# Optimization experiments

Hardware: AMD Instinct MI355X
Metric: run time of the kernel (lower is better)

The kernel has to match this reference:

```python
import jax, jax.numpy as jnp
import numpy as np

N, E, D = 100000, 1600000, 128
BN_EPS = 1e-5


def setup_inputs() -> dict:
    key = jax.random.key(0)
    k0, k1, k2 = jax.random.split(key, 3)
    x = jax.random.normal(k0, (N, D), dtype=jnp.float32)
    edge_index = jax.random.randint(k1, (2, E), 0, N, dtype=jnp.int32)
    # GCNConv weight (glorot-ish scale) and bias
    W = jax.random.normal(k2, (D, D), dtype=jnp.float32) * (1.0 / np.sqrt(D))
    b = jnp.zeros((D,), dtype=jnp.float32)
    # BatchNorm1d affine params
    gamma = jnp.ones((D,), dtype=jnp.float32)
    beta = jnp.zeros((D,), dtype=jnp.float32)
    # PReLU single shared slope (torch default init 0.25)
    a_prelu = jnp.asarray(0.25, dtype=jnp.float32)
    return {"x": x, "W": W, "b": b, "gamma": gamma, "beta": beta,
            "a_prelu": a_prelu, "edge_index": edge_index}


def reference(x, W, b, gamma, beta, a_prelu, edge_index):
    n = x.shape[0]
    loops = jnp.arange(n, dtype=edge_index.dtype)
    src = jnp.concatenate([edge_index[0], loops])  # [E+N]
    dst = jnp.concatenate([edge_index[1], loops])  # [E+N]

    # GCN symmetric normalization with self-loops: deg counts incoming edges
    deg = jax.ops.segment_sum(jnp.ones_like(dst, dtype=x.dtype), dst, num_segments=n)
    dinv = jax.lax.rsqrt(deg)  # deg >= 1 thanks to self-loops
    enorm = dinv[src] * dinv[dst]  # [E+N]

    xw = x @ W                                        # [N, D] transform first
    msg = xw[src] * enorm[:, None]                    # gather + scale
    out = jax.ops.segment_sum(msg, dst, num_segments=n) + b  # scatter-add

    # BatchNorm1d over nodes (training-mode batch statistics, biased var)
    mean = jnp.mean(out, axis=0)
    var = jnp.mean(jnp.square(out - mean), axis=0)
    out = (out - mean) * jax.lax.rsqrt(var + BN_EPS) * gamma + beta

    # PReLU (single shared slope); dropout is identity in eval mode
    out = jnp.where(out > 0, out, a_prelu * out)

    # identity residual (in_dim == out_dim)
    return out + x
```

## Files before the change

kernel.cpp:

```cpp
#include <hip/hip_runtime.h>

#define DIM 128
#define BSH 7
#define BUCK 128
#define CAP2 3072
#define CSH 11
#define CPB 16
#define BINCH 2048
#define MAXC 128

typedef __attribute__((ext_vector_type(8))) short bf16x8;
typedef __attribute__((ext_vector_type(4))) float f32x4;
union U8 { uint4 u; bf16x8 b; };

static __device__ __forceinline__ unsigned f2bf_bits(float f) {
  unsigned u = __float_as_uint(f);
  return (u + 0x7fffu + ((u >> 16) & 1u)) >> 16;
}
static __device__ __forceinline__ unsigned packbf(float a, float b) {
  return (f2bf_bits(a) & 0xffffu) | (f2bf_bits(b) << 16);
}
static __device__ __forceinline__ float bfu_lo(unsigned pk) { return __uint_as_float(pk << 16); }
static __device__ __forceinline__ float bfu_hi(unsigned pk) { return __uint_as_float(pk & 0xffff0000u); }

static __device__ __forceinline__ int eread(const int* __restrict__ e, long long idx, int fl64) {
  return fl64 ? e[idx * 2] : e[idx];
}

__global__ void k_probe(const int* __restrict__ eidx, int* __restrict__ iflag) {
  int lane = threadIdx.x;
  int w = eidx[lane * 2 + 1];
  unsigned long long m = __ballot(w == 0);
  if (lane == 0) *iflag = (__popcll(m) >= 48) ? 1 : 0;
}

__global__ __launch_bounds__(256) void k_prep(const int* __restrict__ eidx, int E,
                                              const int* __restrict__ iflag,
                                              int* __restrict__ c1cnt,
                                              unsigned* __restrict__ tmp1, int CAP1,
                                              int nc,
                                              const float* __restrict__ W,
                                              unsigned* __restrict__ wbt,
                                              int NBB) {
  __shared__ int hist[MAXC];
  __shared__ int lcur[MAXC];
  int bid = blockIdx.x;
  int tid = threadIdx.x;

  if (bid < NBB) {
    int fl = *iflag;
    long long ebase = (long long)bid * BINCH;
    for (int i = tid; i < nc; i += 256) hist[i] = 0;
    __syncthreads();
    unsigned pk[BINCH / 256];
    int bb[BINCH / 256];
#pragma unroll
    for (int it = 0; it < BINCH / 256; ++it) {
      long long e = ebase + it * 256 + tid;
      bb[it] = -1;
      if (e < E) {
        int s = eread(eidx, e, fl);
        int d = eread(eidx, (long long)E + e, fl);
        bb[it] = d >> CSH;
        pk[it] = ((unsigned)s << CSH) | (unsigned)(d & ((1 << CSH) - 1));
        atomicAdd(&hist[bb[it]], 1);
      }
    }
    __syncthreads();
    for (int b = tid; b < nc; b += 256) {
      int h = hist[b];
      lcur[b] = h ? atomicAdd(&c1cnt[b], h) : 0;
    }
    __syncthreads();
#pragma unroll
    for (int it = 0; it < BINCH / 256; ++it) {
      if (bb[it] >= 0) {
        int sl = atomicAdd(&lcur[bb[it]], 1);
        if (sl < CAP1) tmp1[(unsigned)bb[it] * CAP1 + sl] = pk[it];
      }
    }
  } else {
    int w = (bid - NBB) * 256 + tid;
    int c = w >> 6, kk = w & 63;
    float lo = W[(unsigned)(2 * kk) * DIM + c];
    float hi = W[(unsigned)(2 * kk + 1) * DIM + c];
    wbt[(unsigned)c * 64 + kk] = packbf(lo, hi);
  }
}

__global__ __launch_bounds__(256) void k_mid(const int* __restrict__ c1cnt,
                                             const unsigned* __restrict__ tmp1, int CAP1,
                                             int* __restrict__ bcnt,
                                             unsigned* __restrict__ tmp2, int CHK) {
  __shared__ int hist[CPB];
  __shared__ int lcur[CPB];
  int bid = blockIdx.x, tid = threadIdx.x;
  int c = bid / CHK, ch = bid - c * CHK;
  int cnt1 = c1cnt[c]; if (cnt1 > CAP1) cnt1 = CAP1;
  int lo = ch * BINCH;
  int hi = lo + BINCH < cnt1 ? lo + BINCH : cnt1;
  if (tid < CPB) hist[tid] = 0;
  __syncthreads();
  unsigned p2[BINCH / 256];
  int fs[BINCH / 256];
#pragma unroll
  for (int it = 0; it < BINCH / 256; ++it) {
    int j = lo + it * 256 + tid;
    fs[it] = -1;
    if (j < hi) {
      unsigned pk1 = tmp1[(unsigned)c * CAP1 + j];
      fs[it] = (pk1 >> BSH) & (CPB - 1);
      p2[it] = ((pk1 >> CSH) << BSH) | (pk1 & (BUCK - 1));
      atomicAdd(&hist[fs[it]], 1);
    }
  }
  __syncthreads();
  if (tid < CPB) {
    int h = hist[tid];
    lcur[tid] = h ? atomicAdd(&bcnt[c * CPB + tid], h) : 0;
  }
  __syncthreads();
#pragma unroll
  for (int it = 0; it < BINCH / 256; ++it) {
    if (fs[it] >= 0) {
      int sl = atomicAdd(&lcur[fs[it]], 1);
      if (sl < CAP2) tmp2[(unsigned)(c * CPB + fs[it]) * CAP2 + sl] = p2[it];
    }
  }
}

__global__ __launch_bounds__(256) void k_histpack(const int* __restrict__ bcnt,
                                                  const unsigned* __restrict__ tmp2,
                                                  const float* __restrict__ x,
                                                  unsigned* __restrict__ xb, int n) {
  __shared__ int hist[BUCK];
  __shared__ float dls[BUCK];
  int b = blockIdx.x, tid = threadIdx.x;
  int cnt = bcnt[b];
  if (cnt > CAP2) cnt = CAP2;
  unsigned base = (unsigned)b * CAP2;
  if (tid < BUCK) hist[tid] = 0;
  __syncthreads();
  for (int j = tid; j < cnt; j += 256)
    atomicAdd(&hist[tmp2[base + j] & (BUCK - 1)], 1);
  __syncthreads();
  if (tid < BUCK) dls[tid] = rsqrtf((float)(hist[tid] + 1));
  __syncthreads();
  int nb0 = b * BUCK;
#pragma unroll
  for (int it = 0; it < 32; ++it) {
    int idx = it * 256 + tid;
    int ln = idx >> 6, p = idx & 63;
    int node = nb0 + ln;
    if (node < n) {
      float di = dls[ln];
      float2 v = *(const float2*)(x + (size_t)node * DIM + p * 2);
      xb[(unsigned)node * 64 + p] = packbf(v.x * di, v.y * di);
    }
  }
}

__global__ __launch_bounds__(512) void k_fagg(const int* __restrict__ bcnt,
                                              const unsigned* __restrict__ tmp2,
                                              const unsigned* __restrict__ xb,
                                              unsigned* __restrict__ agg, int n) {
  __shared__ unsigned srt[CAP2];
  __shared__ int hist[BUCK];
  __shared__ int sc2[BUCK];
  __shared__ int lcur[BUCK];
  int b = blockIdx.x, tid = threadIdx.x;
  int cnt = bcnt[b];
  if (cnt > CAP2) cnt = CAP2;
  unsigned base = (unsigned)b * CAP2;
  if (tid < BUCK) hist[tid] = 0;
  __syncthreads();
  unsigned r[CAP2 / 512];
#pragma unroll
  for (int u = 0; u < CAP2 / 512; ++u) {
    int j = u * 512 + tid;
    r[u] = 0xffffffffu;
    if (j < cnt) {
      r[u] = tmp2[base + j];
      atomicAdd(&hist[r[u] & (BUCK - 1)], 1);
    }
  }
  __syncthreads();
  if (tid < 64) {
    int h0 = hist[tid * 2], h1 = hist[tid * 2 + 1];
    int s = h0 + h1;
    int pre = s;
#pragma unroll
    for (int d = 1; d < 64; d <<= 1) {
      int t = __shfl_up(pre, d);
      if (tid >= d) pre += t;
    }
    pre -= s;
    sc2[tid * 2] = pre;          lcur[tid * 2] = pre;
    sc2[tid * 2 + 1] = pre + h0; lcur[tid * 2 + 1] = pre + h0;
  }
  __syncthreads();
#pragma unroll
  for (int u = 0; u < CAP2 / 512; ++u) {
    if (r[u] != 0xffffffffu) {
      int sl = atomicAdd(&lcur[r[u] & (BUCK - 1)], 1);
      srt[sl] = r[u];
    }
  }
  __syncthreads();
  int wv = tid >> 6, lane = tid & 63;
  for (int ln = wv; ln < BUCK; ln += 8) {
    int node = b * BUCK + ln;
    if (node >= n) break;
    int o = sc2[ln], dg = hist[ln];
    float di = rsqrtf((float)(dg + 1));
    unsigned xp = xb[(unsigned)node * 64 + lane];
    float ax = bfu_lo(xp), ay = bfu_hi(xp);
    int j = o, je = o + dg;
    for (; j + 8 <= je; j += 8) {
      unsigned s0 = srt[j] >> BSH, s1 = srt[j + 1] >> BSH;
      unsigned s2 = srt[j + 2] >> BSH, s3 = srt[j + 3] >> BSH;
      unsigned s4 = srt[j + 4] >> BSH, s5 = srt[j + 5] >> BSH;
      unsigned s6 = srt[j + 6] >> BSH, s7 = srt[j + 7] >> BSH;
      unsigned v0 = xb[s0 * 64 + lane], v1 = xb[s1 * 64 + lane];
      unsigned v2 = xb[s2 * 64 + lane], v3 = xb[s3 * 64 + lane];
      unsigned v4 = xb[s4 * 64 + lane], v5 = xb[s5 * 64 + lane];
      unsigned v6 = xb[s6 * 64 + lane], v7 = xb[s7 * 64 + lane];
      ax += bfu_lo(v0); ay += bfu_hi(v0);
      ax += bfu_lo(v1); ay += bfu_hi(v1);
      ax += bfu_lo(v2); ay += bfu_hi(v2);
      ax += bfu_lo(v3); ay += bfu_hi(v3);
      ax += bfu_lo(v4); ay += bfu_hi(v4);
      ax += bfu_lo(v5); ay += bfu_hi(v5);
      ax += bfu_lo(v6); ay += bfu_hi(v6);
      ax += bfu_lo(v7); ay += bfu_hi(v7);
    }
    for (; j + 2 <= je; j += 2) {
      unsigned s0 = srt[j] >> BSH, s1 = srt[j + 1] >> BSH;
      unsigned v0 = xb[s0 * 64 + lane], v1 = xb[s1 * 64 + lane];
      ax += bfu_lo(v0); ay += bfu_hi(v0);
      ax += bfu_lo(v1); ay += bfu_hi(v1);
    }
    if (j < je) {
      unsigned vv = xb[(srt[j] >> BSH) * 64 + lane];
      ax += bfu_lo(vv); ay += bfu_hi(vv);
    }
    agg[(unsigned)node * 64 + lane] = packbf(ax * di, ay * di);
  }
}

__global__ __launch_bounds__(256) void k_gemm(
    const unsigned* __restrict__ agg, const unsigned* __restrict__ wbt,
    const float* __restrict__ bias, unsigned* __restrict__ preb,
    float* __restrict__ part, int n) {
  __shared__ unsigned SM[64 * 68 + 128 * 68];
  unsigned* As2 = SM;
  unsigned* WsT = SM + 64 * 68;
  int tid = threadIdx.x;
  int base = blockIdx.x * 64;

#pragma unroll
  for (int it = 0; it < 32; ++it) {
    int idx = it * 256 + tid;
    int c = idx >> 6, kk = idx & 63;
    WsT[c * 68 + kk] = wbt[idx];
  }
#pragma unroll
  for (int it = 0; it < 16; ++it) {
    int idx = it * 256 + tid;
    int rl = idx >> 6, c2 = idx & 63;
    int g = base + rl; if (g >= n) g = n - 1;
    As2[rl * 68 + c2] = agg[(unsigned)g * 64 + c2];
  }
  __syncthreads();

  int w = tid >> 6, l = tid & 63;
  int lg = l >> 4, lr = l & 15;
  f32x4 acc[8];
#pragma unroll
  for (int nt = 0; nt < 8; ++nt) acc[nt] = (f32x4){0.f, 0.f, 0.f, 0.f};

#pragma unroll
  for (int kt = 0; kt < 4; ++kt) {
    U8 bfr;
    bfr.u = *(const uint4*)&As2[(w * 16 + lr) * 68 + kt * 16 + lg * 4];
#pragma unroll
    for (int nt = 0; nt < 8; ++nt) {
      U8 afr;
      afr.u = *(const uint4*)&WsT[(nt * 16 + lr) * 68 + kt * 16 + lg * 4];
      acc[nt] = __builtin_amdgcn_mfma_f32_16x16x32_bf16(afr.b, bfr.b, acc[nt], 0, 0, 0);
    }
  }
  __syncthreads();

  float* Cf = (float*)SM;
#pragma unroll
  for (int nt = 0; nt < 8; ++nt) {
    *(f32x4*)&Cf[(w * 16 + lr) * 132 + nt * 16 + lg * 4] = acc[nt];
  }
  __syncthreads();

  float* bn = Cf + 64 * 132;
  int c2 = tid & 63, g4 = tid >> 6;
  float b0 = bias[2 * c2], b1 = bias[2 * c2 + 1];
  float cs0 = 0.f, cs1 = 0.f, cq0 = 0.f, cq1 = 0.f;
#pragma unroll
  for (int it = 0; it < 16; ++it) {
    int m = it * 4 + g4;
    int gg = base + m;
    float2 vv = *(const float2*)&Cf[m * 132 + 2 * c2];
    float v0 = vv.x + b0, v1 = vv.y + b1;
    if (gg < n) {
      preb[(unsigned)gg * 64 + c2] = packbf(v0, v1);
      cs0 += v0; cq0 += v0 * v0;
      cs1 += v1; cq1 += v1 * v1;
    }
  }
  bn[g4 * 256 + 2 * c2] = cs0;
  bn[g4 * 256 + 2 * c2 + 1] = cs1;
  bn[g4 * 256 + 128 + 2 * c2] = cq0;
  bn[g4 * 256 + 128 + 2 * c2 + 1] = cq1;
  __syncthreads();
  part[(size_t)blockIdx.x * 256 + tid] = bn[tid] + bn[256 + tid] + bn[512 + tid] + bn[768 + tid];
}

__global__ __launch_bounds__(256) void k_redbn(const float* __restrict__ part, int nb,
                                               const float* __restrict__ gma,
                                               const float* __restrict__ bta,
                                               float* __restrict__ sc_,
                                               float* __restrict__ sh_, float invn) {
  __shared__ float r1[256], r2[256];
  int c = blockIdx.x, t = threadIdx.x;
  float s = 0.f, q = 0.f;
  for (int i = t; i < nb; i += 256) {
    s += part[(size_t)i * 256 + c];
    q += part[(size_t)i * 256 + 128 + c];
  }
  r1[t] = s; r2[t] = q;
  __syncthreads();
  for (int k = 128; k > 0; k >>= 1) {
    if (t < k) { r1[t] += r1[t + k]; r2[t] += r2[t + k]; }
    __syncthreads();
  }
  if (t == 0) {
    float mean = r1[0] * invn;
    float var = r2[0] * invn - mean * mean;
    float inv = rsqrtf(var + 1e-5f);
    float g = gma[c] * inv;
    sc_[c] = g;
    sh_[c] = bta[c] - mean * g;
  }
}

__global__ __launch_bounds__(256) void k_final(const unsigned* __restrict__ preb,
                                               const float* __restrict__ x,
                                               const float* __restrict__ sc,
                                               const float* __restrict__ sh,
                                               const float* __restrict__ apre,
                                               float* __restrict__ out, int n) {
  int t = blockIdx.x * 256 + threadIdx.x;
  int i = t >> 6, p = t & 63;
  if (i >= n) return;
  float a = apre[0];
  int c = p * 2;
  unsigned pk = preb[(unsigned)i * 64 + p];
  float t0 = bfu_lo(pk) * sc[c] + sh[c];
  float t1 = bfu_hi(pk) * sc[c + 1] + sh[c + 1];
  t0 = t0 > 0.f ? t0 : a * t0;
  t1 = t1 > 0.f ? t1 : a * t1;
  float2 xv = *(const float2*)(x + (size_t)i * DIM + c);
  t0 += xv.x;
  t1 += xv.y;
  *(float2*)(out + (size_t)i * DIM + c) = make_float2(t0, t1);
}

extern "C" void kernel_launch(void* const* d_in, const int* in_sizes, int n_in,
                              void* d_out, int out_size, void* d_ws, size_t ws_size,
                              hipStream_t stream) {
  (void)n_in; (void)out_size; (void)ws_size;
  const float* x    = (const float*)d_in[0];
  const float* W    = (const float*)d_in[1];
  const float* b    = (const float*)d_in[2];
  const float* gma  = (const float*)d_in[3];
  const float* bta  = (const float*)d_in[4];
  const float* apre = (const float*)d_in[5];
  const int* eidx   = (const int*)d_in[6];
  float* out        = (float*)d_out;

  const int N = in_sizes[0] / DIM;
  const int E = in_sizes[6] / 2;
  const int NB = (N + 63) / 64;
  const int NC = (N + (1 << CSH) - 1) >> CSH;
  const int NBUCK = (N + BUCK - 1) >> BSH;
  const int NBA = NC * CPB;
  const int NBB = (E + BINCH - 1) / BINCH;
  const int NWT = 32;
  int mean1 = E / NC;
  int CHK = (mean1 + mean1 / 8 + 2048 + BINCH - 1) / BINCH;
  const int CAP1 = CHK * BINCH;

  char* wsb = (char*)d_ws;
  size_t off_b = 0;
  auto take = [&](size_t bytes) -> void* {
    void* p = wsb + off_b;
    off_b += (bytes + 255) & ~(size_t)255;
    return p;
  };
  int*      iflag = (int*)     take(256);
  int*      c1cnt = (int*)     take((size_t)(NC + NBA) * 4);
  int*      bcnt  = c1cnt + NC;
  unsigned* wbt   = (unsigned*)take((size_t)DIM * 64 * 4);
  unsigned* tmp1  = (unsigned*)take((size_t)NC * CAP1 * 4);
  unsigned* tmp2  = (unsigned*)take((size_t)NBA * CAP2 * 4);
  unsigned* xb    = (unsigned*)take((size_t)N * 64 * 4);
  unsigned* agg   = (unsigned*)take((size_t)N * 64 * 4);
  float*    part  = (float*)   take((size_t)NB * 256 * 4);
  float*    sc    = (float*)   take(DIM * 4);
  float*    sh    = (float*)   take(DIM * 4);
  unsigned* preb  = agg;

  hipMemsetAsync(c1cnt, 0, (size_t)(NC + NBA) * 4, stream);

  k_probe    <<<1, 64, 0, stream>>>(eidx, iflag);
  k_prep     <<<NBB + NWT, 256, 0, stream>>>(eidx, E, iflag, c1cnt, tmp1, CAP1, NC, W, wbt, NBB);
  k_mid      <<<NC * CHK, 256, 0, stream>>>(c1cnt, tmp1, CAP1, bcnt, tmp2, CHK);
  k_histpack <<<NBUCK, 256, 0, stream>>>(bcnt, tmp2, x, xb, N);
  k_fagg     <<<NBUCK, 512, 0, stream>>>(bcnt, tmp2, xb, agg, N);
  k_gemm     <<<NB, 256, 0, stream>>>(agg, wbt, b, preb, part, N);
  k_redbn    <<<DIM, 256, 0, stream>>>(part, NB, gma, bta, sc, sh, 1.0f / (float)N);
  k_final    <<<(N * 64 + 255) / 256, 256, 0, stream>>>(preb, x, sc, sh, apre, out, N);
}
```

Measured before the change: 275.7 us.

## Move bucket sort into histpack and aggregate one node per wave with 16B gathers

The per-bucket counting sort moves from the aggregation kernel into the earlier hist/pack kernel. The sorted edges are written back to global memory together with a per-node offset and degree. Aggregation becomes a light kernel with one wave per node: four groups of 16 lanes each gather a different neighbour row with uint4 loads, and the partial sums are reduced across groups with xor shuffles. This removes the redundant second histogram/sort pass, spreads the irregular gather work evenly across waves, and widens the loads. The separate probe kernel is folded into k_prep, so every block recomputes the index-width flag. The cost is an extra global write and read of the sorted edge list, plus wasted lanes when a node's degree is not a multiple of four.

```diff
diff --git a/kernel.cpp b/kernel.cpp
--- a/kernel.cpp
+++ b/kernel.cpp
@@ -8,6 +8,7 @@
 #define CPB 16
 #define BINCH 2048
 #define MAXC 128
+#define FPT 12
 
 typedef __attribute__((ext_vector_type(8))) short bf16x8;
 typedef __attribute__((ext_vector_type(4))) float f32x4;
@@ -27,15 +28,7 @@
   return fl64 ? e[idx * 2] : e[idx];
 }
 
-__global__ void k_probe(const int* __restrict__ eidx, int* __restrict__ iflag) {
-  int lane = threadIdx.x;
-  int w = eidx[lane * 2 + 1];
-  unsigned long long m = __ballot(w == 0);
-  if (lane == 0) *iflag = (__popcll(m) >= 48) ? 1 : 0;
-}
-
 __global__ __launch_bounds__(256) void k_prep(const int* __restrict__ eidx, int E,
-                                              const int* __restrict__ iflag,
                                               int* __restrict__ c1cnt,
                                               unsigned* __restrict__ tmp1, int CAP1,
                                               int nc,
@@ -44,14 +37,20 @@
                                               int NBB) {
   __shared__ int hist[MAXC];
   __shared__ int lcur[MAXC];
+  __shared__ int sfl;
   int bid = blockIdx.x;
   int tid = threadIdx.x;
 
   if (bid < NBB) {
-    int fl = *iflag;
-    long long ebase = (long long)bid * BINCH;
+    if (tid < 64) {
+      int w = eidx[tid * 2 + 1];
+      unsigned long long m = __ballot(w == 0);
+      if (tid == 0) sfl = (__popcll(m) >= 48) ? 1 : 0;
+    }
     for (int i = tid; i < nc; i += 256) hist[i] = 0;
     __syncthreads();
+    int fl = sfl;
+    long long ebase = (long long)bid * BINCH;
     unsigned pk[BINCH / 256];
     int bb[BINCH / 256];
 #pragma unroll
@@ -129,11 +128,16 @@
   }
 }
 
-__global__ __launch_bounds__(256) void k_histpack(const int* __restrict__ bcnt,
-                                                  const unsigned* __restrict__ tmp2,
+__global__ __launch_bounds__(256) void k_histsort(const int* __restrict__ bcnt,
+                                                  unsigned* __restrict__ tmp2,
+                                                  int* __restrict__ ofs2,
+                                                  int* __restrict__ deg,
                                                   const float* __restrict__ x,
                                                   unsigned* __restrict__ xb, int n) {
+  __shared__ unsigned srt[CAP2];
   __shared__ int hist[BUCK];
+  __shared__ int sc2[BUCK];
+  __shared__ int lcur[BUCK];
   __shared__ float dls[BUCK];
   int b = blockIdx.x, tid = threadIdx.x;
   int cnt = bcnt[b];
@@ -141,11 +145,52 @@
   unsigned base = (unsigned)b * CAP2;
   if (tid < BUCK) hist[tid] = 0;
   __syncthreads();
-  for (int j = tid; j < cnt; j += 256)
-    atomicAdd(&hist[tmp2[base + j] & (BUCK - 1)], 1);
-  __syncthreads();
+  unsigned r[FPT];
+#pragma unroll
+  for (int u = 0; u < FPT; ++u) {
+    int j = u * 256 + tid;
+    r[u] = 0xffffffffu;
+    if (j < cnt) {
+      r[u] = tmp2[base + j];
+      atomicAdd(&hist[r[u] & (BUCK - 1)], 1);
+    }
+  }
+  __syncthreads();
+  if (tid < 64) {
+    int h0 = hist[tid * 2], h1 = hist[tid * 2 + 1];
+    int s = h0 + h1;
+    int pre = s;
+#pragma unroll
+    for (int d = 1; d < 64; d <<= 1) {
+      int t = __shfl_up(pre, d);
+      if (tid >= d) pre += t;
+    }
+    pre -= s;
+    sc2[tid * 2] = pre;          lcur[tid * 2] = pre;
+    sc2[tid * 2 + 1] = pre + h0; lcur[tid * 2 + 1] = pre + h0;
+  }
+  __syncthreads();
+#pragma unroll
+  for (int u = 0; u < FPT; ++u) {
+    if (r[u] != 0xffffffffu) {
+      int sl = atomicAdd(&lcur[r[u] & (BUCK - 1)], 1);
+      srt[sl] = r[u];
+    }
+  }
   if (tid < BUCK) dls[tid] = rsqrtf((float)(hist[tid] + 1));
   __syncthreads();
+#pragma unroll
+  for (int u = 0; u < FPT; ++u) {
+    int j = u * 256 + tid;
+    if (j < cnt) tmp2[base + j] = srt[j];
+  }
+  if (tid < BUCK) {
+    int node = b * BUCK + tid;
+    if (node < n) {
+      ofs2[node] = (int)base + sc2[tid];
+      deg[node] = hist[tid];
+    }
+  }
   int nb0 = b * BUCK;
 #pragma unroll
   for (int it = 0; it < 32; ++it) {
@@ -160,91 +205,54 @@
   }
 }
 
-__global__ __launch_bounds__(512) void k_fagg(const int* __restrict__ bcnt,
-                                              const unsigned* __restrict__ tmp2,
-                                              const unsigned* __restrict__ xb,
-                                              unsigned* __restrict__ agg, int n) {
-  __shared__ unsigned srt[CAP2];
-  __shared__ int hist[BUCK];
-  __shared__ int sc2[BUCK];
-  __shared__ int lcur[BUCK];
-  int b = blockIdx.x, tid = threadIdx.x;
-  int cnt = bcnt[b];
-  if (cnt > CAP2) cnt = CAP2;
-  unsigned base = (unsigned)b * CAP2;
-  if (tid < BUCK) hist[tid] = 0;
-  __syncthreads();
-  unsigned r[CAP2 / 512];
-#pragma unroll
-  for (int u = 0; u < CAP2 / 512; ++u) {
-    int j = u * 512 + tid;
-    r[u] = 0xffffffffu;
-    if (j < cnt) {
-      r[u] = tmp2[base + j];
-      atomicAdd(&hist[r[u] & (BUCK - 1)], 1);
-    }
-  }
-  __syncthreads();
-  if (tid < 64) {
-    int h0 = hist[tid * 2], h1 = hist[tid * 2 + 1];
-    int s = h0 + h1;
-    int pre = s;
-#pragma unroll
-    for (int d = 1; d < 64; d <<= 1) {
-      int t = __shfl_up(pre, d);
-      if (tid >= d) pre += t;
-    }
-    pre -= s;
-    sc2[tid * 2] = pre;          lcur[tid * 2] = pre;
-    sc2[tid * 2 + 1] = pre + h0; lcur[tid * 2 + 1] = pre + h0;
-  }
-  __syncthreads();
-#pragma unroll
-  for (int u = 0; u < CAP2 / 512; ++u) {
-    if (r[u] != 0xffffffffu) {
-      int sl = atomicAdd(&lcur[r[u] & (BUCK - 1)], 1);
-      srt[sl] = r[u];
-    }
-  }
-  __syncthreads();
-  int wv = tid >> 6, lane = tid & 63;
-  for (int ln = wv; ln < BUCK; ln += 8) {
-    int node = b * BUCK + ln;
-    if (node >= n) break;
-    int o = sc2[ln], dg = hist[ln];
-    float di = rsqrtf((float)(dg + 1));
-    unsigned xp = xb[(unsigned)node * 64 + lane];
-    float ax = bfu_lo(xp), ay = bfu_hi(xp);
-    int j = o, je = o + dg;
-    for (; j + 8 <= je; j += 8) {
-      unsigned s0 = srt[j] >> BSH, s1 = srt[j + 1] >> BSH;
-      unsigned s2 = srt[j + 2] >> BSH, s3 = srt[j + 3] >> BSH;
-      unsigned s4 = srt[j + 4] >> BSH, s5 = srt[j + 5] >> BSH;
-      unsigned s6 = srt[j + 6] >> BSH, s7 = srt[j + 7] >> BSH;
-      unsigned v0 = xb[s0 * 64 + lane], v1 = xb[s1 * 64 + lane];
-      unsigned v2 = xb[s2 * 64 + lane], v3 = xb[s3 * 64 + lane];
-      unsigned v4 = xb[s4 * 64 + lane], v5 = xb[s5 * 64 + lane];
-      unsigned v6 = xb[s6 * 64 + lane], v7 = xb[s7 * 64 + lane];
-      ax += bfu_lo(v0); ay += bfu_hi(v0);
-      ax += bfu_lo(v1); ay += bfu_hi(v1);
-      ax += bfu_lo(v2); ay += bfu_hi(v2);
-      ax += bfu_lo(v3); ay += bfu_hi(v3);
-      ax += bfu_lo(v4); ay += bfu_hi(v4);
-      ax += bfu_lo(v5); ay += bfu_hi(v5);
-      ax += bfu_lo(v6); ay += bfu_hi(v6);
-      ax += bfu_lo(v7); ay += bfu_hi(v7);
-    }
-    for (; j + 2 <= je; j += 2) {
-      unsigned s0 = srt[j] >> BSH, s1 = srt[j + 1] >> BSH;
-      unsigned v0 = xb[s0 * 64 + lane], v1 = xb[s1 * 64 + lane];
-      ax += bfu_lo(v0); ay += bfu_hi(v0);
-      ax += bfu_lo(v1); ay += bfu_hi(v1);
-    }
-    if (j < je) {
-      unsigned vv = xb[(srt[j] >> BSH) * 64 + lane];
-      ax += bfu_lo(vv); ay += bfu_hi(vv);
-    }
-    agg[(unsigned)node * 64 + lane] = packbf(ax * di, ay * di);
+__global__ __launch_bounds__(256) void k_agg(const unsigned* __restrict__ tmp2,
+                                             const unsigned* __restrict__ xb,
+                                             const int* __restrict__ ofs2,
+                                             const int* __restrict__ deg,
+                                             unsigned* __restrict__ agg, int n) {
+  int wid = blockIdx.x * 4 + (threadIdx.x >> 6);
+  if (wid >= n) return;
+  int lane = threadIdx.x & 63;
+  int g = lane >> 4, sl = lane & 15;
+  int e0 = __builtin_amdgcn_readfirstlane(ofs2[wid]);
+  int dg = __builtin_amdgcn_readfirstlane(deg[wid]);
+  float di = rsqrtf((float)(dg + 1));
+  uint4 xp = *(const uint4*)&xb[(unsigned)wid * 64 + sl * 4];
+  float a0, a1, a2, a3, a4, a5, a6, a7;
+  if (g == 0) {
+    a0 = bfu_lo(xp.x); a1 = bfu_hi(xp.x); a2 = bfu_lo(xp.y); a3 = bfu_hi(xp.y);
+    a4 = bfu_lo(xp.z); a5 = bfu_hi(xp.z); a6 = bfu_lo(xp.w); a7 = bfu_hi(xp.w);
+  } else {
+    a0 = a1 = a2 = a3 = a4 = a5 = a6 = a7 = 0.f;
+  }
+  int e1 = e0 + dg;
+#pragma unroll 4
+  for (int j = e0; j < e1; j += 4) {
+    int jj = j + g;
+    bool act = jj < e1;
+    unsigned pk = tmp2[(unsigned)(act ? jj : e0)];
+    unsigned s = pk >> BSH;
+    uint4 v = *(const uint4*)&xb[s * 64 + sl * 4];
+    if (act) {
+      a0 += bfu_lo(v.x); a1 += bfu_hi(v.x); a2 += bfu_lo(v.y); a3 += bfu_hi(v.y);
+      a4 += bfu_lo(v.z); a5 += bfu_hi(v.z); a6 += bfu_lo(v.w); a7 += bfu_hi(v.w);
+    }
+  }
+  a0 += __shfl_xor(a0, 16); a1 += __shfl_xor(a1, 16);
+  a2 += __shfl_xor(a2, 16); a3 += __shfl_xor(a3, 16);
+  a4 += __shfl_xor(a4, 16); a5 += __shfl_xor(a5, 16);
+  a6 += __shfl_xor(a6, 16); a7 += __shfl_xor(a7, 16);
+  a0 += __shfl_xor(a0, 32); a1 += __shfl_xor(a1, 32);
+  a2 += __shfl_xor(a2, 32); a3 += __shfl_xor(a3, 32);
+  a4 += __shfl_xor(a4, 32); a5 += __shfl_xor(a5, 32);
+  a6 += __shfl_xor(a6, 32); a7 += __shfl_xor(a7, 32);
+  if (g == 0) {
+    uint4 o;
+    o.x = packbf(a0 * di, a1 * di);
+    o.y = packbf(a2 * di, a3 * di);
+    o.z = packbf(a4 * di, a5 * di);
+    o.w = packbf(a6 * di, a7 * di);
+    *(uint4*)&agg[(unsigned)wid * 64 + sl * 4] = o;
   }
 }
 
@@ -405,9 +413,10 @@
     off_b += (bytes + 255) & ~(size_t)255;
     return p;
   };
-  int*      iflag = (int*)     take(256);
   int*      c1cnt = (int*)     take((size_t)(NC + NBA) * 4);
   int*      bcnt  = c1cnt + NC;
+  int*      ofs2  = (int*)     take((size_t)N * 4);
+  int*      deg   = (int*)     take((size_t)N * 4);
   unsigned* wbt   = (unsigned*)take((size_t)DIM * 64 * 4);
   unsigned* tmp1  = (unsigned*)take((size_t)NC * CAP1 * 4);
   unsigned* tmp2  = (unsigned*)take((size_t)NBA * CAP2 * 4);
@@ -420,11 +429,10 @@
 
   hipMemsetAsync(c1cnt, 0, (size_t)(NC + NBA) * 4, stream);
 
-  k_probe    <<<1, 64, 0, stream>>>(eidx, iflag);
-  k_prep     <<<NBB + NWT, 256, 0, stream>>>(eidx, E, iflag, c1cnt, tmp1, CAP1, NC, W, wbt, NBB);
+  k_prep     <<<NBB + NWT, 256, 0, stream>>>(eidx, E, c1cnt, tmp1, CAP1, NC, W, wbt, NBB);
   k_mid      <<<NC * CHK, 256, 0, stream>>>(c1cnt, tmp1, CAP1, bcnt, tmp2, CHK);
-  k_histpack <<<NBUCK, 256, 0, stream>>>(bcnt, tmp2, x, xb, N);
-  k_fagg     <<<NBUCK, 512, 0, stream>>>(bcnt, tmp2, xb, agg, N);
+  k_histsort <<<NBUCK, 256, 0, stream>>>(bcnt, tmp2, ofs2, deg, x, xb, N);
+  k_agg      <<<(N + 3) / 4, 256, 0, stream>>>(tmp2, xb, ofs2, deg, agg, N);
   k_gemm     <<<NB, 256, 0, stream>>>(agg, wbt, b, preb, part, N);
   k_redbn    <<<DIM, 256, 0, stream>>>(part, NB, gma, bta, sc, sh, 1.0f / (float)N);
   k_final    <<<(N * 64 + 255) / 256, 256, 0, stream>>>(preb, x, sc, sh, apre, out, N);
```

Measured after the change: 287.0 us. +4.1%, slower.
